# Performance work log

Measured on AMD Instinct MI355X. Metric: run time of the kernel, lower is better.

Reference implementation:

```python
import jax, jax.numpy as jnp
import numpy as np

EPS = 1e-12  # tf.math.l2_normalize epsilon


def get_posenc(n, d):
    # Standard sinusoidal positional encoding, shape [n, d].
    pos = np.arange(n)[:, None].astype(np.float32)
    i = np.arange(d)[None, :]
    angle_rates = 1.0 / np.power(10000.0, (2 * (i // 2)).astype(np.float32) / np.float32(d))
    angles = pos * angle_rates
    pe = np.zeros((n, d), dtype=np.float32)
    pe[:, 0::2] = np.sin(angles[:, 0::2])
    pe[:, 1::2] = np.cos(angles[:, 1::2])
    return jnp.asarray(pe)


def setup_inputs() -> dict:
    key = jax.random.key(0)
    k1, k2, k3 = jax.random.split(key, 3)
    B, N, D = 4, 2048, 2048  # N must equal D (model_size) for the posenc matmul
    data = jax.random.normal(k1, (B, N, D), dtype=jnp.float32)
    W_exp = jax.random.normal(k2, (D + 1, D), dtype=jnp.float32) * (1.0 / np.sqrt(D + 1))
    b_exp = jnp.zeros((D,), dtype=jnp.float32)
    W_merge = jax.random.normal(k3, (2 * D, D), dtype=jnp.float32) * (1.0 / np.sqrt(2 * D))
    return {"data": data, "W_exp": W_exp, "b_exp": b_exp, "W_merge": W_merge}


def reference(data, W_exp, b_exp, W_merge):
    B, N, D = data.shape
    # l2 normalize along feature dim
    sq = jnp.sum(data * data, axis=-1, keepdims=True)
    cn = data * jax.lax.rsqrt(jnp.maximum(sq, EPS))
    # pairwise cosine similarity, rectified: [B, N, N]
    sim = jax.nn.relu(jnp.einsum("bnd,bmd->bnm", cn, cn))
    # fixed positional matmul: posenc [N, D] with D == N -> [B, N, N]
    fixed_v = get_posenc(N, D)
    v_output = jnp.einsum("nk,bkm->bnm", fixed_v, sim)
    # row-sum of similarities: [B, N, 1]
    csum = jnp.sum(sim, axis=-1, keepdims=True)
    counter = jnp.concatenate([csum, v_output], axis=-1)  # [B, N, N+1]
    counter = jax.nn.softplus(counter @ W_exp + b_exp)  # [B, N, D]
    out = jnp.concatenate([data, counter], axis=-1) @ W_merge  # [B, N, D]
    return out
```

## Files before the change

kernel.cpp:

```cpp
#include <hip/hip_runtime.h>

#define B_ 4
#define N_ 2048
#define D_ 2048

#define BM 128
#define BN 128
#define BK 32
#define TP 136

typedef __bf16 bf16x8 __attribute__((ext_vector_type(8)));
typedef float  f32x4  __attribute__((ext_vector_type(4)));

__device__ __forceinline__ ushort f2bf(float x) {
  union { float f; unsigned u; } c; c.f = x;
  unsigned u = c.u;
  u += 0x7fffu + ((u >> 16) & 1u);
  return (ushort)(u >> 16);
}

__device__ __forceinline__ void gld16(ushort* lds, const ushort* g) {
  __builtin_amdgcn_global_load_lds(
      (const __attribute__((address_space(1))) void*)g,
      (__attribute__((address_space(3))) void*)lds, 16, 0, 0);
}


__global__ void prep_cn(const float* __restrict__ data, ushort* __restrict__ cn,
                        ushort* __restrict__ catA) {
  const int row = blockIdx.x;
  const long base = (long)row * D_;
  const float4* r4 = (const float4*)(data + base);
  const int tid = threadIdx.x;
  float4 u0 = r4[tid * 2], u1 = r4[tid * 2 + 1];
  float s = u0.x*u0.x + u0.y*u0.y + u0.z*u0.z + u0.w*u0.w
          + u1.x*u1.x + u1.y*u1.y + u1.z*u1.z + u1.w*u1.w;
  #pragma unroll
  for (int o = 32; o > 0; o >>= 1) s += __shfl_down(s, o);
  __shared__ float wsum[4];
  if ((tid & 63) == 0) wsum[tid >> 6] = s;
  __syncthreads();
  const float tot = wsum[0] + wsum[1] + wsum[2] + wsum[3];
  const float sc = rsqrtf(fmaxf(tot, 1e-12f));
  uint4 pc, pd;
  pc.x = (unsigned)f2bf(u0.x * sc) | ((unsigned)f2bf(u0.y * sc) << 16);
  pc.y = (unsigned)f2bf(u0.z * sc) | ((unsigned)f2bf(u0.w * sc) << 16);
  pc.z = (unsigned)f2bf(u1.x * sc) | ((unsigned)f2bf(u1.y * sc) << 16);
  pc.w = (unsigned)f2bf(u1.z * sc) | ((unsigned)f2bf(u1.w * sc) << 16);
  pd.x = (unsigned)f2bf(u0.x) | ((unsigned)f2bf(u0.y) << 16);
  pd.y = (unsigned)f2bf(u0.z) | ((unsigned)f2bf(u0.w) << 16);
  pd.z = (unsigned)f2bf(u1.x) | ((unsigned)f2bf(u1.y) << 16);
  pd.w = (unsigned)f2bf(u1.z) | ((unsigned)f2bf(u1.w) << 16);
  *(uint4*)(cn + base + tid * 8) = pc;
  *(uint4*)(catA + (long)row * (2 * D_) + tid * 8) = pd;
}

__global__ void prep_pe(ushort* __restrict__ pe) {
  const int id = blockIdx.x * 256 + threadIdx.x;
  const int n = id >> 11, d = id & (D_ - 1);
  const float e = (float)(2 * (d >> 1)) * (1.0f / (float)D_);
  const float rate = expf(e * -9.210340371976184f);
  const float ang = (float)n * rate;
  const float v = (d & 1) ? cosf(ang) : sinf(ang);
  pe[id] = f2bf(v);
}

__global__ void transpose_bf16(const float* __restrict__ in, ushort* __restrict__ out,
                               int R, int C) {
  __shared__ float t[32][33];
  const int c0 = blockIdx.x * 32, r0 = blockIdx.y * 32;
  const int tx = threadIdx.x, ty = threadIdx.y;
  #pragma unroll
  for (int i = 0; i < 32; i += 8) t[ty + i][tx] = in[(long)(r0 + ty + i) * C + c0 + tx];
  __syncthreads();
  #pragma unroll
  for (int i = 0; i < 32; i += 8) out[(long)(c0 + ty + i) * R + r0 + tx] = f2bf(t[tx][ty + i]);
}

__global__ __launch_bounds__(256, 2) void gemm_sym(
    const ushort* __restrict__ Ag, ushort* __restrict__ Cg, float* __restrict__ csum) {
  __shared__ ushort sAt[BM * BK];
  __shared__ ushort sBt[BN * BK];
  __shared__ ushort tile[128 * TP];

  const int bz = blockIdx.z;
  const int t = blockIdx.x;
  int bj = (int)((sqrtf(8.f * (float)t + 1.f) - 1.f) * 0.5f);
  while ((bj + 1) * (bj + 2) / 2 <= t) bj++;
  while (bj * (bj + 1) / 2 > t) bj--;
  const int bi = t - bj * (bj + 1) / 2;

  const ushort* A = Ag + (long)bz * N_ * D_;
  const int blockRow = bi * BM;
  const int blockCol = bj * BN;

  const int tid = threadIdx.x;
  const int w = tid >> 6, L = tid & 63;
  const int ldRow = w * 16 + (L >> 2);
  const int ldK = (((L & 3) ^ ((L >> 3) & 3)) * 8);
  const ushort* a0 = A + (long)(blockRow + ldRow) * D_ + ldK;
  const ushort* a1 = a0 + (long)64 * D_;
  const ushort* b0 = A + (long)(blockCol + ldRow) * D_ + ldK;
  const ushort* b1 = b0 + (long)64 * D_;
  ushort* sA0 = sAt + w * 512;
  ushort* sA1 = sAt + 2048 + w * 512;
  ushort* sB0 = sBt + w * 512;
  ushort* sB1 = sBt + 2048 + w * 512;

  const int wm = (w & 1) * 64, wn = (w >> 1) * 64;
  const int fr = L & 15;
  const int sw = (((L >> 4) ^ ((fr >> 1) & 3)) * 8);

  f32x4 acc[4][4] = {};
  for (int k0 = 0; k0 < D_; k0 += BK) {
    gld16(sA0, a0); gld16(sA1, a1);
    gld16(sB0, b0); gld16(sB1, b1);
    a0 += BK; a1 += BK; b0 += BK; b1 += BK;
    __syncthreads();
    bf16x8 af[4], bfv[4];
    #pragma unroll
    for (int i = 0; i < 4; i++) af[i]  = *(const bf16x8*)&sAt[(wm + i * 16 + fr) * BK + sw];
    #pragma unroll
    for (int j = 0; j < 4; j++) bfv[j] = *(const bf16x8*)&sBt[(wn + j * 16 + fr) * BK + sw];
    #pragma unroll
    for (int i = 0; i < 4; i++)
      #pragma unroll
      for (int j = 0; j < 4; j++)
        acc[i][j] = __builtin_amdgcn_mfma_f32_16x16x32_bf16(af[i], bfv[j], acc[i][j], 0, 0, 0);
    __syncthreads();
  }

  const int rq = (L >> 4) * 4;
  const int cq = L & 15;
  ushort* C = Cg + (long)bz * N_ * N_;

  float rs[4][4];
  float cs[4];
  #pragma unroll
  for (int i = 0; i < 4; i++)
    #pragma unroll
    for (int r = 0; r < 4; r++) rs[i][r] = 0.f;
  #pragma unroll
  for (int j = 0; j < 4; j++) cs[j] = 0.f;

  const bool offdiag = (bi != bj);

  #pragma unroll
  for (int i = 0; i < 4; i++)
    #pragma unroll
    for (int j = 0; j < 4; j++)
      #pragma unroll
      for (int r = 0; r < 4; r++) {
        const float v = fmaxf(acc[i][j][r], 0.f);
        rs[i][r] += v;
        cs[j] += v;
        tile[(wm + i * 16 + rq + r) * TP + wn + j * 16 + cq] = f2bf(v);
      }
  __syncthreads();
  {
    const int rp = tid >> 1, h = tid & 1;
    const ushort* src = &tile[rp * TP + h * 64];
    ushort* dst = &C[(long)(blockRow + rp) * N_ + blockCol + h * 64];
    #pragma unroll
    for (int q = 0; q < 8; q++)
      *(uint4*)(dst + q * 8) = *(const uint4*)(src + q * 8);
  }

  #pragma unroll
  for (int i = 0; i < 4; i++)
    #pragma unroll
    for (int r = 0; r < 4; r++) {
      float s = rs[i][r];
      s += __shfl_xor(s, 1); s += __shfl_xor(s, 2);
      s += __shfl_xor(s, 4); s += __shfl_xor(s, 8);
      if (cq == 0)
        atomicAdd(&csum[(long)bz * N_ + blockRow + wm + i * 16 + rq + r], s);
    }

  if (offdiag) {
    #pragma unroll
    for (int j = 0; j < 4; j++) {
      float s = cs[j];
      s += __shfl_xor(s, 16); s += __shfl_xor(s, 32);
      if (L < 16)
        atomicAdd(&csum[(long)bz * N_ + blockCol + wn + j * 16 + cq], s);
    }
    __syncthreads();
    #pragma unroll
    for (int i = 0; i < 4; i++)
      #pragma unroll
      for (int j = 0; j < 4; j++)
        #pragma unroll
        for (int r = 0; r < 4; r++) {
          const float v = fmaxf(acc[i][j][r], 0.f);
          tile[(wn + j * 16 + cq) * TP + wm + i * 16 + rq + r] = f2bf(v);
        }
    __syncthreads();
    const int rp = tid >> 1, h = tid & 1;
    const ushort* src = &tile[rp * TP + h * 64];
    ushort* dst = &C[(long)(blockCol + rp) * N_ + blockRow + h * 64];
    #pragma unroll
    for (int q = 0; q < 8; q++)
      *(uint4*)(dst + q * 8) = *(const uint4*)(src + q * 8);
  }
}


__device__ __forceinline__ void stage_half(ushort* d, const ushort* s, int K) {
  gld16(d, s);
  gld16(d + 4096, s + (long)64 * K);
}

template <int M0, bool FIRST, class STG>
__device__ __forceinline__ void phase8(const ushort* __restrict__ TA,
                                       const ushort* __restrict__ TB,
                                       int aO0, int aO1, int bO0, int bO1,
                                       bf16x8 (&bf)[4][2], f32x4 (&acc)[8][4],
                                       int vm, STG&& stg) {
  if (FIRST) {
    #pragma unroll
    for (int j = 0; j < 4; j++) {
      bf[j][0] = *(const bf16x8*)&TB[bO0 + j * 1024];
      bf[j][1] = *(const bf16x8*)&TB[bO1 + j * 1024];
    }
  }
  bf16x8 af[2][2];
  #pragma unroll
  for (int mm = 0; mm < 2; mm++) {
    af[mm][0] = *(const bf16x8*)&TA[aO0 + (M0 + mm) * 1024];
    af[mm][1] = *(const bf16x8*)&TA[aO1 + (M0 + mm) * 1024];
  }
  __builtin_amdgcn_sched_barrier(0);
  stg();
  asm volatile("s_barrier" ::: "memory");
  asm volatile("s_waitcnt lgkmcnt(0)" ::: "memory");
  __builtin_amdgcn_sched_barrier(0);
  __builtin_amdgcn_s_setprio(1);
  #pragma unroll
  for (int kk = 0; kk < 2; kk++)
    #pragma unroll
    for (int mm = 0; mm < 2; mm++)
      #pragma unroll
      for (int j = 0; j < 4; j++)
        acc[M0 + mm][j] = __builtin_amdgcn_mfma_f32_16x16x32_bf16(
            af[mm][kk], bf[j][kk], acc[M0 + mm][j], 0, 0, 0);
  __builtin_amdgcn_s_setprio(0);
  if (vm == 6)      asm volatile("s_waitcnt vmcnt(6)" ::: "memory");
  else if (vm == 0) asm volatile("s_waitcnt vmcnt(0)" ::: "memory");
  asm volatile("s_barrier" ::: "memory");
}

template <int MODE>
__global__ __launch_bounds__(512, 2) void gemm8(
    const ushort* __restrict__ Ag, const ushort* __restrict__ Bg, void* __restrict__ Cg,
    int K, long sA, long sB, long sC, int ldc, int colOff,
    const float* __restrict__ csum, const float* __restrict__ w0,
    const float* __restrict__ bexp) {
  extern __shared__ ushort lds[];

  const int lin = blockIdx.x + (blockIdx.y << 3) + (blockIdx.z << 6);
  const int xcd = lin & 7, m_ = lin >> 3;
  const int bz = xcd >> 1;
  const int by = ((xcd & 1) << 2) + (m_ >> 3);
  const int bx = m_ & 7;

  const ushort* A  = Ag + (long)bz * sA + (long)(bx << 8) * K;
  const ushort* Bp = Bg + (long)bz * sB + (long)(by << 8) * K;

  const int tid = threadIdx.x;
  const int sr = tid >> 3;
  const int sc = ((tid & 7) ^ (sr & 7)) << 3;
  const ushort* aS = A + (long)sr * K + sc;
  const ushort* bS = Bp + (long)sr * K + sc;
  const int wOff = (tid >> 6) << 9;
  ushort* const stA0 = lds + wOff;
  ushort* const stA1 = lds + 16384 + wOff;
  ushort* const stB0 = lds + 32768 + wOff;
  ushort* const stB1 = lds + 49152 + wOff;
  const ushort* const TA0 = lds;          const ushort* const TA1 = lds + 16384;
  const ushort* const TB0 = lds + 32768;  const ushort* const TB1 = lds + 49152;

  auto stg = [&](ushort* base, const ushort* src, int T, int H) {
    stage_half(base + (H << 13), src + (long)(H << 7) * K + ((long)T << 6), K);
  };

  const int L = tid & 63, wid = tid >> 6;
  const int wr = wid >> 2, wc = wid & 3;
  const int fr = L & 15, g = L >> 4;
  const int off0 = ((g ^ (fr & 7)) << 3);
  const int aO0 = ((wr << 7) + fr) * 64 + off0, aO1 = aO0 ^ 32;
  const int bO0 = ((wc << 6) + fr) * 64 + off0, bO1 = bO0 ^ 32;

  f32x4 acc[8][4] = {};
  bf16x8 bf[4][2];

  const int NT = K >> 6, NTI = NT >> 1;

  stg(stB0, bS, 0, 0); stg(stB0, bS, 0, 1); stg(stA0, aS, 0, 0); stg(stA0, aS, 0, 1);
  stg(stB1, bS, 1, 0); stg(stB1, bS, 1, 1); stg(stA1, aS, 1, 0); stg(stA1, aS, 1, 1);
  asm volatile("s_waitcnt vmcnt(6)" ::: "memory");
  asm volatile("s_barrier" ::: "memory");

  for (int it = 0; it < NTI; ++it) {
    const int T2 = 2 * it + 2;
    const bool more = (it + 1 < NTI);
    phase8<0, true >(TA0, TB0, aO0, aO1, bO0, bO1, bf, acc, -1, [&] {});
    phase8<2, false>(TA0, TB0, aO0, aO1, bO0, bO1, bf, acc, -1,
                     [&] { if (more) stg(stB0, bS, T2, 0); });
    phase8<4, false>(TA0, TB0, aO0, aO1, bO0, bO1, bf, acc, -1,
                     [&] { if (more) stg(stB0, bS, T2, 1); });
    phase8<6, false>(TA0, TB0, aO0, aO1, bO0, bO1, bf, acc, more ? 6 : 0,
                     [&] { if (more) { stg(stA0, aS, T2, 0); stg(stA0, aS, T2, 1); } });
    phase8<0, true >(TA1, TB1, aO0, aO1, bO0, bO1, bf, acc, -1, [&] {});
    phase8<2, false>(TA1, TB1, aO0, aO1, bO0, bO1, bf, acc, -1,
                     [&] { if (more) stg(stB1, bS, T2 + 1, 0); });
    phase8<4, false>(TA1, TB1, aO0, aO1, bO0, bO1, bf, acc, -1,
                     [&] { if (more) stg(stB1, bS, T2 + 1, 1); });
    phase8<6, false>(TA1, TB1, aO0, aO1, bO0, bO1, bf, acc, more ? 6 : -1,
                     [&] { if (more) { stg(stA1, aS, T2 + 1, 0); stg(stA1, aS, T2 + 1, 1); } });
  }

  const int cq = fr;
  const int rowB0 = (bx << 8) + (wr << 7);
  const int colB0 = (by << 8) + (wc << 6);

  if (MODE == 3) {
    float* eT = (float*)lds + (size_t)wid * 1088;
    float* Cb = (float*)Cg + (long)bz * sC;
    const int er = L >> 4, ec = L & 15;
    #pragma unroll
    for (int m = 0; m < 8; m++) {
      #pragma unroll
      for (int j = 0; j < 4; j++)
        #pragma unroll
        for (int r = 0; r < 4; r++)
          eT[(g * 4 + r) * 68 + j * 16 + cq] = acc[m][j][r];
      #pragma unroll
      for (int q = 0; q < 4; q++) {
        const f32x4 v = *(const f32x4*)&eT[(er + q * 4) * 68 + ec * 4];
        const long row = rowB0 + m * 16 + er + q * 4;
        *(f32x4*)&Cb[row * ldc + colB0 + ec * 4] = v;
      }
    }
  } else {
    ushort* eT = lds + (size_t)wid * 1152;
    ushort* Cb = (ushort*)Cg + (long)bz * sC;
    const int er = L >> 3, ec = L & 7;
    float w0v[4], bev[4];
    if (MODE == 2) {
      #pragma unroll
      for (int j = 0; j < 4; j++) {
        w0v[j] = w0[colB0 + j * 16 + cq];
        bev[j] = bexp[colB0 + j * 16 + cq];
      }
    }
    #pragma unroll
    for (int m = 0; m < 8; m++) {
      #pragma unroll
      for (int j = 0; j < 4; j++)
        #pragma unroll
        for (int r = 0; r < 4; r++) {
          float x = acc[m][j][r];
          if (MODE == 2) {
            const float cv = csum[(long)bz * N_ + rowB0 + m * 16 + g * 4 + r];
            x = x + cv * w0v[j] + bev[j];
            x = fmaxf(x, 0.f) + log1pf(expf(-fabsf(x)));
          }
          eT[(g * 4 + r) * 72 + j * 16 + cq] = f2bf(x);
        }
      #pragma unroll
      for (int q = 0; q < 2; q++) {
        const uint4 v = *(const uint4*)&eT[(er + q * 8) * 72 + ec * 8];
        const long row = rowB0 + m * 16 + er + q * 8;
        *(uint4*)&Cb[row * ldc + colOff + colB0 + ec * 8] = v;
      }
    }
  }
}

extern "C" void kernel_launch(void* const* d_in, const int* in_sizes, int n_in,
                              void* d_out, int out_size, void* d_ws, size_t ws_size,
                              hipStream_t stream) {
  const float* data    = (const float*)d_in[0];
  const float* W_exp   = (const float*)d_in[1];
  const float* b_exp   = (const float*)d_in[2];
  const float* W_merge = (const float*)d_in[3];

  char* ws = (char*)d_ws;
  const size_t MB = 1024 * 1024;
  ushort* cnv  = (ushort*)(ws);
  ushort* sim  = (ushort*)(ws + 32 * MB);
  ushort* pe   = (ushort*)(ws + 64 * MB);
  ushort* weT  = (ushort*)(ws + 72 * MB);
  ushort* wmT  = (ushort*)(ws + 80 * MB);
  ushort* catA = (ushort*)(ws + 96 * MB);
  float*  csum = (float*)(ws + 160 * MB);

  static bool attrs_set = false;
  if (!attrs_set) {
    (void)hipFuncSetAttribute((const void*)gemm8<1>, hipFuncAttributeMaxDynamicSharedMemorySize, 131072);
    (void)hipFuncSetAttribute((const void*)gemm8<2>, hipFuncAttributeMaxDynamicSharedMemorySize, 131072);
    (void)hipFuncSetAttribute((const void*)gemm8<3>, hipFuncAttributeMaxDynamicSharedMemorySize, 131072);
    attrs_set = true;
  }

  hipMemsetAsync(csum, 0, (size_t)B_ * N_ * sizeof(float), stream);
  prep_cn<<<B_ * N_, 256, 0, stream>>>(data, cnv, catA);
  prep_pe<<<(N_ * N_) / 256, 256, 0, stream>>>(pe);
  transpose_bf16<<<dim3(D_ / 32, D_ / 32), dim3(32, 8), 0, stream>>>(W_exp + D_, weT, D_, D_);
  transpose_bf16<<<dim3(D_ / 32, (2 * D_) / 32), dim3(32, 8), 0, stream>>>(W_merge, wmT, 2 * D_, D_);

  gemm_sym<<<dim3(136, 1, B_), dim3(256), 0, stream>>>(cnv, sim, csum);

  dim3 g8(N_ / 256, N_ / 256, B_);
  gemm8<1><<<g8, 512, 131072, stream>>>(pe, sim, cnv, N_, 0, (long)N_ * N_,
                                        (long)N_ * N_, N_, 0, nullptr, nullptr, nullptr);
  gemm8<2><<<g8, 512, 131072, stream>>>(cnv, weT, catA, N_, (long)N_ * N_, 0,
                                        (long)N_ * 2 * D_, 2 * D_, D_, csum, W_exp, b_exp);
  gemm8<3><<<g8, 512, 131072, stream>>>(catA, wmT, d_out, 2 * D_, (long)N_ * 2 * D_, 0,
                                        (long)N_ * D_, D_, 0, nullptr, nullptr, nullptr);
}
```

Measured before the change: 508.0 us.

## Software-pipeline LDS fragment reads one phase ahead of MFMA in GEMM main loop

Restructures the double-buffered GEMM main loop so that the LDS reads of the next A/B fragments are issued right after the current MFMA block rather than before it. Each phase then computes on fragments already in registers. The global-to-LDS staging order is reshuffled so the vmcnt waits line up with the new schedule, and it uses different counts (4 instead of 6). The aim is to hide LDS read latency behind MFMA work and drop one barrier per phase, at the cost of more fragile manual synchronisation.

```diff
diff --git a/kernel.cpp b/kernel.cpp
--- a/kernel.cpp
+++ b/kernel.cpp
@@ -211,31 +211,27 @@
   gld16(d + 4096, s + (long)64 * K);
 }
 
-template <int M0, bool FIRST, class STG>
-__device__ __forceinline__ void phase8(const ushort* __restrict__ TA,
-                                       const ushort* __restrict__ TB,
-                                       int aO0, int aO1, int bO0, int bO1,
-                                       bf16x8 (&bf)[4][2], f32x4 (&acc)[8][4],
-                                       int vm, STG&& stg) {
-  if (FIRST) {
-    #pragma unroll
-    for (int j = 0; j < 4; j++) {
-      bf[j][0] = *(const bf16x8*)&TB[bO0 + j * 1024];
-      bf[j][1] = *(const bf16x8*)&TB[bO1 + j * 1024];
-    }
-  }
-  bf16x8 af[2][2];
-  #pragma unroll
-  for (int mm = 0; mm < 2; mm++) {
-    af[mm][0] = *(const bf16x8*)&TA[aO0 + (M0 + mm) * 1024];
-    af[mm][1] = *(const bf16x8*)&TA[aO1 + (M0 + mm) * 1024];
-  }
-  __builtin_amdgcn_sched_barrier(0);
-  stg();
-  asm volatile("s_barrier" ::: "memory");
-  asm volatile("s_waitcnt lgkmcnt(0)" ::: "memory");
-  __builtin_amdgcn_sched_barrier(0);
-  __builtin_amdgcn_s_setprio(1);
+template <int M0>
+__device__ __forceinline__ void rd_a(const ushort* __restrict__ T, int aO0, int aO1,
+                                     bf16x8 (&af)[2][2]) {
+  af[0][0] = *(const bf16x8*)&T[aO0 + M0 * 1024];
+  af[0][1] = *(const bf16x8*)&T[aO1 + M0 * 1024];
+  af[1][0] = *(const bf16x8*)&T[aO0 + (M0 + 1) * 1024];
+  af[1][1] = *(const bf16x8*)&T[aO1 + (M0 + 1) * 1024];
+}
+
+__device__ __forceinline__ void rd_b8(const ushort* __restrict__ T, int bO0, int bO1,
+                                      bf16x8 (&bf)[4][2]) {
+  #pragma unroll
+  for (int j = 0; j < 4; j++) {
+    bf[j][0] = *(const bf16x8*)&T[bO0 + j * 1024];
+    bf[j][1] = *(const bf16x8*)&T[bO1 + j * 1024];
+  }
+}
+
+template <int M0>
+__device__ __forceinline__ void mfma16(const bf16x8 (&af)[2][2], const bf16x8 (&bf)[4][2],
+                                       f32x4 (&acc)[8][4]) {
   #pragma unroll
   for (int kk = 0; kk < 2; kk++)
     #pragma unroll
@@ -244,11 +240,15 @@
       for (int j = 0; j < 4; j++)
         acc[M0 + mm][j] = __builtin_amdgcn_mfma_f32_16x16x32_bf16(
             af[mm][kk], bf[j][kk], acc[M0 + mm][j], 0, 0, 0);
-  __builtin_amdgcn_s_setprio(0);
-  if (vm == 6)      asm volatile("s_waitcnt vmcnt(6)" ::: "memory");
-  else if (vm == 0) asm volatile("s_waitcnt vmcnt(0)" ::: "memory");
-  asm volatile("s_barrier" ::: "memory");
-}
+}
+
+#define W_LGKM0 asm volatile("s_waitcnt lgkmcnt(0)" ::: "memory")
+#define W_VM4   asm volatile("s_waitcnt vmcnt(4)" ::: "memory")
+#define W_VM0   asm volatile("s_waitcnt vmcnt(0)" ::: "memory")
+#define SBAR    asm volatile("s_barrier" ::: "memory")
+#define SCHB    __builtin_amdgcn_sched_barrier(0)
+#define PRIO1   __builtin_amdgcn_s_setprio(1)
+#define PRIO0   __builtin_amdgcn_s_setprio(0)
 
 template <int MODE>
 __global__ __launch_bounds__(512, 2) void gemm8(
@@ -292,32 +292,72 @@
   const int bO0 = ((wc << 6) + fr) * 64 + off0, bO1 = bO0 ^ 32;
 
   f32x4 acc[8][4] = {};
-  bf16x8 bf[4][2];
+  bf16x8 af[2][2], bf[4][2];
 
   const int NT = K >> 6, NTI = NT >> 1;
 
   stg(stB0, bS, 0, 0); stg(stB0, bS, 0, 1); stg(stA0, aS, 0, 0); stg(stA0, aS, 0, 1);
-  stg(stB1, bS, 1, 0); stg(stB1, bS, 1, 1); stg(stA1, aS, 1, 0); stg(stA1, aS, 1, 1);
+  stg(stB1, bS, 1, 0); stg(stB1, bS, 1, 1);
+  stg(stA1, aS, 1, 0);
   asm volatile("s_waitcnt vmcnt(6)" ::: "memory");
-  asm volatile("s_barrier" ::: "memory");
+  SBAR;
+  rd_b8(TB0, bO0, bO1, bf);
+  rd_a<0>(TA0, aO0, aO1, af);
 
   for (int it = 0; it < NTI; ++it) {
-    const int T2 = 2 * it + 2;
+    const int t1 = 2 * it + 1, t2 = 2 * it + 2, t3 = 2 * it + 3;
     const bool more = (it + 1 < NTI);
-    phase8<0, true >(TA0, TB0, aO0, aO1, bO0, bO1, bf, acc, -1, [&] {});
-    phase8<2, false>(TA0, TB0, aO0, aO1, bO0, bO1, bf, acc, -1,
-                     [&] { if (more) stg(stB0, bS, T2, 0); });
-    phase8<4, false>(TA0, TB0, aO0, aO1, bO0, bO1, bf, acc, -1,
-                     [&] { if (more) stg(stB0, bS, T2, 1); });
-    phase8<6, false>(TA0, TB0, aO0, aO1, bO0, bO1, bf, acc, more ? 6 : 0,
-                     [&] { if (more) { stg(stA0, aS, T2, 0); stg(stA0, aS, T2, 1); } });
-    phase8<0, true >(TA1, TB1, aO0, aO1, bO0, bO1, bf, acc, -1, [&] {});
-    phase8<2, false>(TA1, TB1, aO0, aO1, bO0, bO1, bf, acc, -1,
-                     [&] { if (more) stg(stB1, bS, T2 + 1, 0); });
-    phase8<4, false>(TA1, TB1, aO0, aO1, bO0, bO1, bf, acc, -1,
-                     [&] { if (more) stg(stB1, bS, T2 + 1, 1); });
-    phase8<6, false>(TA1, TB1, aO0, aO1, bO0, bO1, bf, acc, more ? 6 : -1,
-                     [&] { if (more) { stg(stA1, aS, T2 + 1, 0); stg(stA1, aS, T2 + 1, 1); } });
+
+    stg(stA1, aS, t1, 1);
+    W_LGKM0; SCHB;
+    PRIO1; mfma16<0>(af, bf, acc); PRIO0; SCHB;
+    rd_a<2>(TA0, aO0, aO1, af);
+    SBAR;
+    if (more) stg(stB0, bS, t2, 0);
+    W_LGKM0; SCHB;
+    PRIO1; mfma16<2>(af, bf, acc); PRIO0; SCHB;
+    rd_a<4>(TA0, aO0, aO1, af);
+    SBAR;
+    if (more) stg(stB0, bS, t2, 1);
+    W_LGKM0; SCHB;
+    PRIO1; mfma16<4>(af, bf, acc); PRIO0; SCHB;
+    rd_a<6>(TA0, aO0, aO1, af);
+    SBAR;
+    W_LGKM0;
+    if (more) { W_VM4; } else { W_VM0; }
+    SBAR;
+    SCHB;
+    PRIO1; mfma16<6>(af, bf, acc); PRIO0; SCHB;
+    rd_b8(TB1, bO0, bO1, bf);
+    rd_a<0>(TA1, aO0, aO1, af);
+    SBAR;
+    if (more) stg(stA0, aS, t2, 0);
+    W_LGKM0; SCHB;
+    PRIO1; mfma16<0>(af, bf, acc); PRIO0; SCHB;
+    rd_a<2>(TA1, aO0, aO1, af);
+    SBAR;
+    if (more) stg(stA0, aS, t2, 1);
+    W_LGKM0; SCHB;
+    PRIO1; mfma16<2>(af, bf, acc); PRIO0; SCHB;
+    rd_a<4>(TA1, aO0, aO1, af);
+    SBAR;
+    if (more) stg(stB1, bS, t3, 0);
+    W_LGKM0; SCHB;
+    PRIO1; mfma16<4>(af, bf, acc); PRIO0; SCHB;
+    rd_a<6>(TA1, aO0, aO1, af);
+    SBAR;
+    if (more) stg(stB1, bS, t3, 1);
+    W_LGKM0;
+    if (more) { W_VM4; }
+    SBAR;
+    SCHB;
+    PRIO1; mfma16<6>(af, bf, acc); PRIO0; SCHB;
+    if (more) {
+      rd_b8(TB0, bO0, bO1, bf);
+      rd_a<0>(TA0, aO0, aO1, af);
+      stg(stA1, aS, t3, 0);
+    }
+    SBAR;
   }
 
   const int cq = fr;
```

Result: no change. 500.2 us (-1.5%).
